# Kernel tuning notes

Measured on AMD Instinct MI355X. Metric: run time of the kernel, lower is better.

Reference implementation:

```python
import jax, jax.numpy as jnp
import numpy as np

B, C, H, W = 8, 256, 128, 128
SH, SW = 8, 8            # stoken_size
HH, WW = H // SH, W // SW
NH = 8                   # num_heads
HD = C // NH             # head_dim = 32
KD = HD                  # key_dim (attn_ratio=1)
ATTN_SCALE = KD ** (-0.5)
AFF_SCALE = C ** (-0.5)


def unfold9(x):
    """x: (B,C,hh,ww) -> (B, hh*ww, C, 9); matches Unfold(3) + transpose/reshape."""
    b, c, hh, ww = x.shape
    xp = jnp.pad(x, ((0, 0), (0, 0), (1, 1), (1, 1)))
    p = jnp.stack([xp[:, :, dy:dy + hh, dx:dx + ww]
                   for dy in range(3) for dx in range(3)], axis=2)  # (B,C,9,hh,ww)
    return p.transpose(0, 3, 4, 1, 2).reshape(b, hh * ww, c, 9)


def fold9(y):
    """y: (B,C,9,hh,ww) -> (B,C,hh,ww); matches Fold(3) (conv_transpose with identity kernels)."""
    hh, ww = y.shape[-2:]
    yp = jnp.pad(y, ((0, 0), (0, 0), (0, 0), (1, 1), (1, 1)))
    out = 0.
    for dy in range(3):
        for dx in range(3):
            out = out + yp[:, :, dy * 3 + dx, 2 - dy:2 - dy + hh, 2 - dx:2 - dx + ww]
    return out


def attention(sf, w_qkv, w_pe, w_proj):
    """Attention module with attn_ratio=1 (Conv layers have act=False, BN identity)."""
    b, c, hh, ww = sf.shape
    n = hh * ww
    qkv = jnp.einsum('oc,bchw->bohw', w_qkv, sf).reshape(b, NH, 2 * KD + HD, n)
    q, k, v = jnp.split(qkv, [KD, 2 * KD], axis=2)
    attn = jax.nn.softmax(jnp.einsum('bhkn,bhkm->bhnm', q, k) * ATTN_SCALE, axis=-1)
    o = jnp.einsum('bhdm,bhnm->bhdn', v, attn).reshape(b, c, hh, ww)
    pe = jax.lax.conv_general_dilated(
        v.reshape(b, c, hh, ww), w_pe, (1, 1), ((1, 1), (1, 1)),
        dimension_numbers=('NCHW', 'OIHW', 'NCHW'), feature_group_count=c)
    return jnp.einsum('oc,bchw->bohw', w_proj, o + pe)


def setup_inputs() -> dict:
    key = jax.random.key(0)
    k0, k1, k2, k3 = jax.random.split(key, 4)
    x = jax.random.normal(k0, (B, C, H, W), dtype=jnp.float32)
    w_qkv = jax.random.normal(k1, (3 * C, C), dtype=jnp.float32) * 0.05
    w_pe = jax.random.normal(k2, (C, 1, 3, 3), dtype=jnp.float32) * 0.05
    w_proj = jax.random.normal(k3, (C, C), dtype=jnp.float32) * 0.05
    return {'x': x, 'w_qkv': w_qkv, 'w_pe': w_pe, 'w_proj': w_proj}


def reference(x, w_qkv, w_pe, w_proj):
    # H,W divisible by stoken_size -> no padding branch
    xb = x.reshape(B, C, HH, SH, WW, SW)
    stoken = xb.mean(axis=(3, 5))                                   # (B,C,hh,ww) adaptive_avg_pool2d
    pix = xb.transpose(0, 2, 4, 3, 5, 1).reshape(B, HH * WW, SH * SW, C)
    # --- single no-grad iteration (n_iter=1) ---
    sf9 = unfold9(stoken)                                            # (B,n,C,9)
    aff = jax.nn.softmax(jnp.einsum('bnpc,bnck->bnpk', pix, sf9) * AFF_SCALE, axis=-1)
    aff = jax.lax.stop_gradient(aff)                                 # torch.no_grad
    asum = aff.sum(axis=2).transpose(0, 2, 1).reshape(B, 1, 9, HH, WW)
    asum = jax.lax.stop_gradient(fold9(asum))                        # (B,1,hh,ww)
    # --- super-token aggregation ---
    sf = jnp.einsum('bnpc,bnpk->bnck', pix, aff)                     # (B,n,C,9)
    sf = fold9(sf.transpose(0, 2, 3, 1).reshape(B, C, 9, HH, WW))    # (B,C,hh,ww)
    sf = sf / (asum + 1e-12)
    # --- refine with attention ---
    sf = attention(sf, w_qkv, w_pe, w_proj)
    # --- scatter back to pixels ---
    sf9b = unfold9(sf)                                               # (B,n,C,9)
    pix_out = jnp.einsum('bnck,bnpk->bnpc', sf9b, aff)               # (B,n,h*w,C)
    return pix_out.reshape(B, HH, WW, C, SH, SW).transpose(0, 3, 1, 4, 2, 5).reshape(B, C, H, W)
```

## Files before the change

kernel.cpp:

```cpp
#include <hip/hip_runtime.h>
#include <cstdint>
#include <cstddef>


#define AFF_SCALE 0.0625f
#define ATTN_SCALE 0.17677669529663687f

__global__ __launch_bounds__(128) void stoken_kernel(
    const float* __restrict__ x, float* __restrict__ stok_pad)
{
    int blk = blockIdx.x;
    int i  = blk & 15;
    int bc = blk >> 4;
    int t  = threadIdx.x;
    const float* xr = x + ((size_t)bc * 128 + i * 8) * 128 + t;
    float s = 0.f;
#pragma unroll
    for (int r = 0; r < 8; ++r) s += xr[r * 128];
    s += __shfl_down(s, 4, 64);
    s += __shfl_down(s, 2, 64);
    s += __shfl_down(s, 1, 64);
    if ((t & 7) == 0) {
        int j = t >> 3;
        int b = bc >> 8, c = bc & 255;
        stok_pad[(((size_t)b * 18 + (i + 1)) * 18 + (j + 1)) * 256 + c] =
            s * (1.f / 64.f);
    }
}

__global__ __launch_bounds__(256) void aff_agg_kernel(
    const float* __restrict__ x, const float* __restrict__ stok_pad,
    float* __restrict__ aff_g, float* __restrict__ asum_g,
    float* __restrict__ agg)
{
    __shared__ __align__(16) float pixs[256 * 68];
    __shared__ __align__(16) float sfs[9 * 260];
    __shared__ __align__(16) float part[576];

    int bid  = blockIdx.x;
    int xcd  = bid & 7, slot_ = bid >> 3;
    int pair = xcd * 128 + (slot_ >> 1);
    int m = pair & 7, i = (pair >> 3) & 15, b = pair >> 7;
    int j = m * 2 + (slot_ & 1);
    int bn = b * 256 + i * 16 + j;
    int t = threadIdx.x;

    {
        int c0 = t >> 3, pi = t & 7;
#pragma unroll
        for (int it = 0; it < 8; ++it) {
            int c = c0 + 32 * it;
            const float* xp = x + (((size_t)b * 256 + c) * 128 + i * 8 + pi) * 128 + j * 8;
            float4 f0 = *(const float4*)&xp[0];
            float4 f1 = *(const float4*)&xp[4];
            int gma = (c >> 2) & 3;
            int s0 = (2 * pi) ^ gma, s1 = (2 * pi + 1) ^ gma;
            *(float4*)&pixs[c * 68 + s0 * 4] = f0;
            *(float4*)&pixs[c * 68 + s1 * 4] = f1;
        }
    }
    {
        const float* spT = stok_pad + (size_t)b * 324 * 256;
#pragma unroll
        for (int dy = 0; dy < 3; ++dy)
#pragma unroll
            for (int dx = 0; dx < 3; ++dx)
                sfs[(dy * 3 + dx) * 260 + t] =
                    spT[((size_t)(i + dy) * 18 + (j + dx)) * 256 + t];
    }
    part[t] = 0.f;
    part[t + 256] = 0.f;
    if (t < 64) part[t + 512] = 0.f;
    __syncthreads();

    int w = t >> 6, l = t & 63;

    {
        int pq = l >> 2, cgl = l & 3;
        int cbase = w * 64 + cgl * 16;
        float acc[4][9];
#pragma unroll
        for (int ii = 0; ii < 4; ++ii)
#pragma unroll
            for (int k = 0; k < 9; ++k) acc[ii][k] = 0.f;

#pragma unroll
        for (int c4i = 0; c4i < 4; ++c4i) {
            int c = cbase + c4i * 4;
            int slot = (pq ^ c4i) * 4;
            const float4 p0 = *(const float4*)&pixs[(c + 0) * 68 + slot];
            const float4 p1 = *(const float4*)&pixs[(c + 1) * 68 + slot];
            const float4 p2 = *(const float4*)&pixs[(c + 2) * 68 + slot];
            const float4 p3 = *(const float4*)&pixs[(c + 3) * 68 + slot];
#pragma unroll
            for (int k = 0; k < 9; ++k) {
                const float4 sv = *(const float4*)&sfs[k * 260 + c];
                acc[0][k] += p0.x * sv.x + p1.x * sv.y + p2.x * sv.z + p3.x * sv.w;
                acc[1][k] += p0.y * sv.x + p1.y * sv.y + p2.y * sv.z + p3.y * sv.w;
                acc[2][k] += p0.z * sv.x + p1.z * sv.y + p2.z * sv.z + p3.z * sv.w;
                acc[3][k] += p0.w * sv.x + p1.w * sv.y + p2.w * sv.z + p3.w * sv.w;
            }
        }
#pragma unroll
        for (int ii = 0; ii < 4; ++ii)
#pragma unroll
            for (int k = 0; k < 9; ++k) {
                acc[ii][k] += __shfl_xor(acc[ii][k], 1, 64);
                acc[ii][k] += __shfl_xor(acc[ii][k], 2, 64);
            }
#pragma unroll
        for (int k = 0; k < 9; ++k) {
            float v01 = (cgl & 1) ? acc[1][k] : acc[0][k];
            float v23 = (cgl & 1) ? acc[3][k] : acc[2][k];
            float vk  = (cgl & 2) ? v23 : v01;
            atomicAdd(&part[l * 9 + k], vk);
        }
    }
    __syncthreads();

    float* affs = sfs;

    if (t < 64) {
        float a[9];
        float mx = -1e30f;
#pragma unroll
        for (int k = 0; k < 9; ++k) {
            float v = part[t * 9 + k] * AFF_SCALE;
            a[k] = v;
            mx = fmaxf(mx, v);
        }
        float ssum = 0.f;
#pragma unroll
        for (int k = 0; k < 9; ++k) { a[k] = __expf(a[k] - mx); ssum += a[k]; }
        float inv = 1.f / ssum;
#pragma unroll
        for (int k = 0; k < 9; ++k) {
            a[k] *= inv;
            affs[k * 64 + t] = a[k];
            aff_g[(size_t)bn * 576 + k * 64 + t] = a[k];
        }
#pragma unroll
        for (int k = 0; k < 9; ++k) {
            float r = a[k];
            r += __shfl_down(r, 32, 64); r += __shfl_down(r, 16, 64);
            r += __shfl_down(r, 8, 64);  r += __shfl_down(r, 4, 64);
            r += __shfl_down(r, 2, 64);  r += __shfl_down(r, 1, 64);
            if (t == 0) asum_g[(size_t)bn * 9 + k] = r;
        }
    }
    __syncthreads();

    {
        int cql = l >> 2, pq2 = l & 3;
        int cb2 = w * 64 + cql * 4;
        int gma = cql & 3;
        float acc2[4][9];
#pragma unroll
        for (int ii = 0; ii < 4; ++ii)
#pragma unroll
            for (int k = 0; k < 9; ++k) acc2[ii][k] = 0.f;

#pragma unroll
        for (int pp = 0; pp < 4; ++pp) {
            int p4 = pq2 * 4 + pp;
            int slot = (p4 ^ gma) * 4;
            const float4 q0 = *(const float4*)&pixs[(cb2 + 0) * 68 + slot];
            const float4 q1 = *(const float4*)&pixs[(cb2 + 1) * 68 + slot];
            const float4 q2 = *(const float4*)&pixs[(cb2 + 2) * 68 + slot];
            const float4 q3 = *(const float4*)&pixs[(cb2 + 3) * 68 + slot];
#pragma unroll
            for (int k = 0; k < 9; ++k) {
                const float4 av = *(const float4*)&affs[k * 64 + p4 * 4];
                acc2[0][k] += q0.x * av.x + q0.y * av.y + q0.z * av.z + q0.w * av.w;
                acc2[1][k] += q1.x * av.x + q1.y * av.y + q1.z * av.z + q1.w * av.w;
                acc2[2][k] += q2.x * av.x + q2.y * av.y + q2.z * av.z + q2.w * av.w;
                acc2[3][k] += q3.x * av.x + q3.y * av.y + q3.z * av.z + q3.w * av.w;
            }
        }
#pragma unroll
        for (int ii = 0; ii < 4; ++ii)
#pragma unroll
            for (int k = 0; k < 9; ++k) {
                acc2[ii][k] += __shfl_xor(acc2[ii][k], 1, 64);
                acc2[ii][k] += __shfl_xor(acc2[ii][k], 2, 64);
            }
        int cout = w * 64 + l;
#pragma unroll
        for (int k = 0; k < 9; ++k) {
            float v01 = (pq2 & 1) ? acc2[1][k] : acc2[0][k];
            float v23 = (pq2 & 1) ? acc2[3][k] : acc2[2][k];
            float vk  = (pq2 & 2) ? v23 : v01;
            agg[((size_t)bn * 9 + k) * 256 + cout] = vk;
        }
    }
}

__global__ __launch_bounds__(256) void fold_div_kernel(
    const float* __restrict__ agg, const float* __restrict__ asum_g,
    float* __restrict__ sf)
{
    __shared__ float v[256 * 17];
    int b = blockIdx.x >> 4, y = blockIdx.x & 15;
    int t = threadIdx.x;
    for (int x = 0; x < 16; ++x) {
        float af = 0.f, val = 0.f;
#pragma unroll
        for (int dy = 0; dy < 3; ++dy)
#pragma unroll
            for (int dx = 0; dx < 3; ++dx) {
                int ii = y + 1 - dy, jj = x + 1 - dx;
                if ((unsigned)ii < 16u && (unsigned)jj < 16u) {
                    int idx = (b * 256 + ii * 16 + jj) * 9 + dy * 3 + dx;
                    af  += asum_g[idx];
                    val += agg[(size_t)idx * 256 + t];
                }
            }
        v[t * 17 + x] = val / (af + 1e-12f);
    }
    __syncthreads();
    int xw = t & 15, cw0 = t >> 4;
#pragma unroll
    for (int it = 0; it < 16; ++it) {
        int c = cw0 + it * 16;
        sf[((size_t)b * 256 + c) * 256 + y * 16 + xw] = v[c * 17 + xw];
    }
}

__global__ __launch_bounds__(256) void gemm_w(
    const float* __restrict__ A, const float* __restrict__ Bm,
    float* __restrict__ Cout, int M, int mode)
{
    __shared__ float As[32 * 68];
    __shared__ float Bs[32 * 64];
    int b = blockIdx.x, o0 = blockIdx.y * 64, n0 = blockIdx.z * 64;
    int t = threadIdx.x;
    int tr = t >> 4, tc = t & 15;
    const float* Bb = Bm + (size_t)b * 256 * 256;
    float acc[4][4];
#pragma unroll
    for (int ii = 0; ii < 4; ++ii)
#pragma unroll
        for (int jj = 0; jj < 4; ++jj) acc[ii][jj] = 0.f;

    for (int k0 = 0; k0 < 256; k0 += 32) {
        {
            int ol = t >> 2, kq = (t & 3) * 8;
            const float* Ap = A + (size_t)(o0 + ol) * 256 + k0 + kq;
            const float4 f0 = *(const float4*)&Ap[0];
            const float4 f1 = *(const float4*)&Ap[4];
            As[(kq + 0) * 68 + ol] = f0.x; As[(kq + 1) * 68 + ol] = f0.y;
            As[(kq + 2) * 68 + ol] = f0.z; As[(kq + 3) * 68 + ol] = f0.w;
            As[(kq + 4) * 68 + ol] = f1.x; As[(kq + 5) * 68 + ol] = f1.y;
            As[(kq + 6) * 68 + ol] = f1.z; As[(kq + 7) * 68 + ol] = f1.w;
        }
#pragma unroll
        for (int i2 = 0; i2 < 8; ++i2) {
            int e = t + i2 * 256;
            int kl = e >> 6, nl = e & 63;
            Bs[kl * 64 + nl] = Bb[(size_t)(k0 + kl) * 256 + n0 + nl];
        }
        __syncthreads();
#pragma unroll
        for (int kk = 0; kk < 32; ++kk) {
            const float4 av = *(const float4*)&As[kk * 68 + tr * 4];
            const float4 bv = *(const float4*)&Bs[kk * 64 + tc * 4];
            acc[0][0] += av.x * bv.x; acc[0][1] += av.x * bv.y; acc[0][2] += av.x * bv.z; acc[0][3] += av.x * bv.w;
            acc[1][0] += av.y * bv.x; acc[1][1] += av.y * bv.y; acc[1][2] += av.y * bv.z; acc[1][3] += av.y * bv.w;
            acc[2][0] += av.z * bv.x; acc[2][1] += av.z * bv.y; acc[2][2] += av.z * bv.z; acc[2][3] += av.z * bv.w;
            acc[3][0] += av.w * bv.x; acc[3][1] += av.w * bv.y; acc[3][2] += av.w * bv.z; acc[3][3] += av.w * bv.w;
        }
        __syncthreads();
    }

    if (mode == 0) {
#pragma unroll
        for (int ii = 0; ii < 4; ++ii) {
            int o = o0 + tr * 4 + ii;
            float4 st = make_float4(acc[ii][0], acc[ii][1], acc[ii][2], acc[ii][3]);
            *(float4*)&Cout[((size_t)b * M + o) * 256 + n0 + tc * 4] = st;
        }
    } else {
#pragma unroll
        for (int jj = 0; jj < 4; ++jj) {
            int n = n0 + tc * 4 + jj;
            int y = n >> 4, x = n & 15;
            float4 st = make_float4(acc[0][jj], acc[1][jj], acc[2][jj], acc[3][jj]);
            *(float4*)&Cout[(((size_t)b * 18 + 1 + y) * 18 + 1 + x) * 256 + o0 + tr * 4] = st;
        }
    }
}

__global__ __launch_bounds__(256) void attn_kernel(
    const float* __restrict__ qkv, float* __restrict__ o_attn)
{
    __shared__ float smem[9216];
    int b = blockIdx.x, h = blockIdx.y, nt = blockIdx.z;
    int t = threadIdx.x, nl = t & 63, mq = t >> 6;
    int n = nt * 64 + nl;

    {
        int dd = t >> 3, mb = (t & 7) * 32;
        const float* krow = qkv + ((size_t)b * 768 + h * 96 + 32 + dd) * 256;
#pragma unroll
        for (int e4 = 0; e4 < 8; ++e4) {
            int m = mb + e4 * 4;
            const float4 kw = *(const float4*)&krow[m];
            smem[(m + 0) * 32 + dd] = kw.x; smem[(m + 1) * 32 + dd] = kw.y;
            smem[(m + 2) * 32 + dd] = kw.z; smem[(m + 3) * 32 + dd] = kw.w;
        }
    }
    float q[32];
    {
        const float* qbase = qkv + ((size_t)b * 768 + h * 96) * 256 + n;
#pragma unroll
        for (int d = 0; d < 32; ++d) q[d] = qbase[(size_t)d * 256];
    }
    __syncthreads();

    float l[64];
#pragma unroll
    for (int e = 0; e < 64; ++e) {
        const float* kp = &smem[(mq * 64 + e) * 32];
        float s = 0.f;
#pragma unroll
        for (int d4 = 0; d4 < 8; ++d4) {
            const float4 kv4 = *(const float4*)&kp[d4 * 4];
            s += q[d4 * 4 + 0] * kv4.x + q[d4 * 4 + 1] * kv4.y +
                 q[d4 * 4 + 2] * kv4.z + q[d4 * 4 + 3] * kv4.w;
        }
        l[e] = s * ATTN_SCALE;
    }
    float mx = -1e30f;
#pragma unroll
    for (int e = 0; e < 64; ++e) mx = fmaxf(mx, l[e]);
    float sm = 0.f;
#pragma unroll
    for (int e = 0; e < 64; ++e) { l[e] = __expf(l[e] - mx); sm += l[e]; }
    __syncthreads();

    {
        int dd = t >> 3, mb = (t & 7) * 32;
        const float* vrow = qkv + ((size_t)b * 768 + h * 96 + 64 + dd) * 256;
#pragma unroll
        for (int e4 = 0; e4 < 8; ++e4) {
            int m = mb + e4 * 4;
            const float4 vw = *(const float4*)&vrow[m];
            smem[(m + 0) * 32 + dd] = vw.x; smem[(m + 1) * 32 + dd] = vw.y;
            smem[(m + 2) * 32 + dd] = vw.z; smem[(m + 3) * 32 + dd] = vw.w;
        }
    }
    __syncthreads();

    float oa[32];
#pragma unroll
    for (int d = 0; d < 32; ++d) oa[d] = 0.f;
#pragma unroll
    for (int e = 0; e < 64; ++e) {
        float pm = l[e];
        const float* vp = &smem[(mq * 64 + e) * 32];
#pragma unroll
        for (int d4 = 0; d4 < 8; ++d4) {
            const float4 vv = *(const float4*)&vp[d4 * 4];
            oa[d4 * 4 + 0] += pm * vv.x; oa[d4 * 4 + 1] += pm * vv.y;
            oa[d4 * 4 + 2] += pm * vv.z; oa[d4 * 4 + 3] += pm * vv.w;
        }
    }
    __syncthreads();

    float* op   = smem;
    float* mxsm = smem + 8448;
    {
        int idx = mq * 64 + nl;
#pragma unroll
        for (int d = 0; d < 32; ++d) op[idx * 33 + d] = oa[d];
        mxsm[idx * 2 + 0] = mx;
        mxsm[idx * 2 + 1] = sm;
    }
    __syncthreads();

    if (t < 64) {
        float M2 = -1e30f;
#pragma unroll
        for (int q4 = 0; q4 < 4; ++q4) M2 = fmaxf(M2, mxsm[(q4 * 64 + t) * 2]);
        float w[4], S = 0.f;
#pragma unroll
        for (int q4 = 0; q4 < 4; ++q4) {
            w[q4] = __expf(mxsm[(q4 * 64 + t) * 2] - M2);
            S += mxsm[(q4 * 64 + t) * 2 + 1] * w[q4];
        }
        float inv = 1.f / S;
#pragma unroll
        for (int d = 0; d < 32; ++d) {
            float o = 0.f;
#pragma unroll
            for (int q4 = 0; q4 < 4; ++q4) o += op[(q4 * 64 + t) * 33 + d] * w[q4];
            o_attn[((size_t)b * 256 + h * 32 + d) * 256 + nt * 64 + t] = o * inv;
        }
    }
}

__global__ __launch_bounds__(256) void peadd_kernel(
    const float* __restrict__ qkv, const float* __restrict__ w_pe,
    float* __restrict__ o_attn)
{
    int bc = blockIdx.x;
    int b = bc >> 8, c = bc & 255;
    int t = threadIdx.x;
    int y = t >> 4, x = t & 15;
    int h = c >> 5, d = c & 31;
    const float* v = qkv + ((size_t)b * 768 + h * 96 + 64 + d) * 256;
    float acc = o_attn[(size_t)bc * 256 + t];
#pragma unroll
    for (int ky = 0; ky < 3; ++ky)
#pragma unroll
        for (int kx = 0; kx < 3; ++kx) {
            int yy = y + ky - 1, xx = x + kx - 1;
            if ((unsigned)yy < 16u && (unsigned)xx < 16u)
                acc += w_pe[c * 9 + ky * 3 + kx] * v[yy * 16 + xx];
        }
    o_attn[(size_t)bc * 256 + t] = acc;
}

__global__ __launch_bounds__(256) void scatter_kernel(
    const float* __restrict__ sfa_pad, const float* __restrict__ aff_g,
    float* __restrict__ out)
{
    __shared__ float ss[3 * 18 * 40];
    __shared__ float aff_s[16 * 577];

    int blk = blockIdx.x;
    int pi = blk & 7, i = (blk >> 3) & 15, b = blk >> 7;
    int t = threadIdx.x;

    for (int e = t; e < 1728; e += 256) {
        int dy = e / 576, rem = e % 576;
        int col = rem >> 5, idx = rem & 31;
        int q = idx >> 3, d = idx & 7;
        ss[(dy * 18 + col) * 40 + idx] =
            sfa_pad[(((size_t)b * 18 + i + dy) * 18 + col) * 256 + q * 64 + pi * 8 + d];
    }
    {
        const float* ag = aff_g + ((size_t)b * 256 + i * 16) * 576;
        for (int e = t; e < 9216; e += 256) {
            int j = e / 576, rem = e % 576;
            int k = rem >> 6, p = rem & 63;
            aff_s[j * 577 + p * 9 + k] = ag[j * 576 + rem];
        }
    }
    __syncthreads();

    int lane = t & 63, w = t >> 6;
    int j0 = lane >> 3, pj = lane & 7;
    int j1 = j0 + 8;

    float S0[4][9], S1[4][9];
#pragma unroll
    for (int q = 0; q < 4; ++q)
#pragma unroll
        for (int k = 0; k < 9; ++k) {
            int dy = k / 3, dx = k % 3;
            S0[q][k] = ss[(dy * 18 + j0 + dx) * 40 + q * 8 + pj];
            S1[q][k] = ss[(dy * 18 + j1 + dx) * 40 + q * 8 + pj];
        }

    int y = i * 8 + pi;
    size_t ob = (size_t)b * 256 * 16384 + (size_t)y * 128;
    const float* A0 = &aff_s[j0 * 577];
    const float* A1 = &aff_s[j1 * 577];
    for (int p = w * 16; p < w * 16 + 16; ++p) {
        float a0[9], a1[9];
#pragma unroll
        for (int k = 0; k < 9; ++k) { a0[k] = A0[p * 9 + k]; a1[k] = A1[p * 9 + k]; }
#pragma unroll
        for (int q = 0; q < 4; ++q) {
            int c2 = p * 4 + q;
            float v0 = 0.f, v1 = 0.f;
#pragma unroll
            for (int k = 0; k < 9; ++k) {
                v0 += S0[q][k] * a0[k];
                v1 += S1[q][k] * a1[k];
            }
            out[ob + (size_t)c2 * 16384 + lane] = v0;
            out[ob + (size_t)c2 * 16384 + 64 + lane] = v1;
        }
    }
}

extern "C" void kernel_launch(void* const* d_in, const int* in_sizes, int n_in,
                              void* d_out, int out_size, void* d_ws, size_t ws_size,
                              hipStream_t stream) {
    const float* x      = (const float*)d_in[0];
    const float* w_qkv  = (const float*)d_in[1];
    const float* w_pe   = (const float*)d_in[2];
    const float* w_proj = (const float*)d_in[3];
    float* out = (float*)d_out;
    float* agg = (float*)d_out;

    float* ws = (float*)d_ws;
    const size_t o_aff  = 0;
    const size_t o_asum = 1179648;
    const size_t o_pad  = 1198080;
    const size_t o_sf   = 1861632;
    const size_t o_qkv  = 2385920;

    hipMemsetAsync(ws + o_pad, 0, 663552 * sizeof(float), stream);

    stoken_kernel<<<8 * 256 * 16, 128, 0, stream>>>(x, ws + o_pad);
    aff_agg_kernel<<<8 * 256, 256, 0, stream>>>(x, ws + o_pad, ws + o_aff,
                                                ws + o_asum, agg);
    fold_div_kernel<<<8 * 16, 256, 0, stream>>>(agg, ws + o_asum, ws + o_sf);
    gemm_w<<<dim3(8, 12, 4), 256, 0, stream>>>(w_qkv, ws + o_sf, ws + o_qkv, 768, 0);
    hipMemsetAsync(ws + o_pad, 0, 663552 * sizeof(float), stream);
    attn_kernel<<<dim3(8, 8, 4), 256, 0, stream>>>(ws + o_qkv, ws + o_sf);
    peadd_kernel<<<8 * 256, 256, 0, stream>>>(ws + o_qkv, w_pe, ws + o_sf);
    gemm_w<<<dim3(8, 4, 4), 256, 0, stream>>>(w_proj, ws + o_sf, ws + o_pad, 256, 1);
    scatter_kernel<<<8 * 16 * 8, 256, 0, stream>>>(ws + o_pad, ws + o_aff, out);
}
```

Measured before the change: 442.9 us.

## Split affinity/aggregation kernel, read pixels from global, drop pad memsets

The fused affinity+aggregation kernel is split into two kernels that each read pixel data directly from global memory instead of staging a 68KB shared tile, with launch bounds requesting 4 blocks per SM to raise occupancy. The two memsets of the padded buffer are removed and replaced by bounds checks on the halo reads in the affinity and scatter kernels. Cross-lane reductions use DPP intrinsics instead of shuffles. The trade-off is that x is read twice from global/L2 and there is one extra kernel launch.

New measurement: 442.1 us. Within noise of the previous version (-0.2%).

```diff
diff --git a/kernel.cpp b/kernel.cpp
--- a/kernel.cpp
+++ b/kernel.cpp
@@ -5,6 +5,15 @@
 
 #define AFF_SCALE 0.0625f
 #define ATTN_SCALE 0.17677669529663687f
+
+__device__ __forceinline__ float dpp_add_xor1(float v) {
+    int p = __builtin_amdgcn_update_dpp(0, __float_as_int(v), 0xB1, 0xF, 0xF, true);
+    return v + __int_as_float(p);
+}
+__device__ __forceinline__ float dpp_add_xor2(float v) {
+    int p = __builtin_amdgcn_update_dpp(0, __float_as_int(v), 0x4E, 0xF, 0xF, true);
+    return v + __int_as_float(p);
+}
 
 __global__ __launch_bounds__(128) void stoken_kernel(
     const float* __restrict__ x, float* __restrict__ stok_pad)
@@ -28,12 +37,10 @@
     }
 }
 
-__global__ __launch_bounds__(256) void aff_agg_kernel(
+__global__ __launch_bounds__(256, 4) void aff_kernel(
     const float* __restrict__ x, const float* __restrict__ stok_pad,
-    float* __restrict__ aff_g, float* __restrict__ asum_g,
-    float* __restrict__ agg)
-{
-    __shared__ __align__(16) float pixs[256 * 68];
+    float* __restrict__ aff_g, float* __restrict__ asum_g)
+{
     __shared__ __align__(16) float sfs[9 * 260];
     __shared__ __align__(16) float part[576];
 
@@ -46,27 +53,17 @@
     int t = threadIdx.x;
 
     {
-        int c0 = t >> 3, pi = t & 7;
-#pragma unroll
-        for (int it = 0; it < 8; ++it) {
-            int c = c0 + 32 * it;
-            const float* xp = x + (((size_t)b * 256 + c) * 128 + i * 8 + pi) * 128 + j * 8;
-            float4 f0 = *(const float4*)&xp[0];
-            float4 f1 = *(const float4*)&xp[4];
-            int gma = (c >> 2) & 3;
-            int s0 = (2 * pi) ^ gma, s1 = (2 * pi + 1) ^ gma;
-            *(float4*)&pixs[c * 68 + s0 * 4] = f0;
-            *(float4*)&pixs[c * 68 + s1 * 4] = f1;
-        }
-    }
-    {
         const float* spT = stok_pad + (size_t)b * 324 * 256;
 #pragma unroll
         for (int dy = 0; dy < 3; ++dy)
 #pragma unroll
-            for (int dx = 0; dx < 3; ++dx)
-                sfs[(dy * 3 + dx) * 260 + t] =
-                    spT[((size_t)(i + dy) * 18 + (j + dx)) * 256 + t];
+            for (int dx = 0; dx < 3; ++dx) {
+                int r = i + dy, cn = j + dx;
+                float v = 0.f;
+                if ((unsigned)(r - 1) < 16u && (unsigned)(cn - 1) < 16u)
+                    v = spT[((size_t)r * 18 + cn) * 256 + t];
+                sfs[(dy * 3 + dx) * 260 + t] = v;
+            }
     }
     part[t] = 0.f;
     part[t + 256] = 0.f;
@@ -74,10 +71,12 @@
     __syncthreads();
 
     int w = t >> 6, l = t & 63;
-
     {
         int pq = l >> 2, cgl = l & 3;
         int cbase = w * 64 + cgl * 16;
+        int pi = pq >> 1, pj4 = (pq & 1) * 4;
+        const float* xb = x + (size_t)(b * 256) * 16384
+                            + (size_t)(i * 8 + pi) * 128 + j * 8 + pj4;
         float acc[4][9];
 #pragma unroll
         for (int ii = 0; ii < 4; ++ii)
@@ -87,11 +86,10 @@
 #pragma unroll
         for (int c4i = 0; c4i < 4; ++c4i) {
             int c = cbase + c4i * 4;
-            int slot = (pq ^ c4i) * 4;
-            const float4 p0 = *(const float4*)&pixs[(c + 0) * 68 + slot];
-            const float4 p1 = *(const float4*)&pixs[(c + 1) * 68 + slot];
-            const float4 p2 = *(const float4*)&pixs[(c + 2) * 68 + slot];
-            const float4 p3 = *(const float4*)&pixs[(c + 3) * 68 + slot];
+            const float4 p0 = *(const float4*)&xb[(size_t)(c + 0) * 16384];
+            const float4 p1 = *(const float4*)&xb[(size_t)(c + 1) * 16384];
+            const float4 p2 = *(const float4*)&xb[(size_t)(c + 2) * 16384];
+            const float4 p3 = *(const float4*)&xb[(size_t)(c + 3) * 16384];
 #pragma unroll
             for (int k = 0; k < 9; ++k) {
                 const float4 sv = *(const float4*)&sfs[k * 260 + c];
@@ -105,8 +103,8 @@
         for (int ii = 0; ii < 4; ++ii)
 #pragma unroll
             for (int k = 0; k < 9; ++k) {
-                acc[ii][k] += __shfl_xor(acc[ii][k], 1, 64);
-                acc[ii][k] += __shfl_xor(acc[ii][k], 2, 64);
+                acc[ii][k] = dpp_add_xor1(acc[ii][k]);
+                acc[ii][k] = dpp_add_xor2(acc[ii][k]);
             }
 #pragma unroll
         for (int k = 0; k < 9; ++k) {
@@ -118,8 +116,6 @@
     }
     __syncthreads();
 
-    float* affs = sfs;
-
     if (t < 64) {
         float a[9];
         float mx = -1e30f;
@@ -136,7 +132,6 @@
 #pragma unroll
         for (int k = 0; k < 9; ++k) {
             a[k] *= inv;
-            affs[k * 64 + t] = a[k];
             aff_g[(size_t)bn * 576 + k * 64 + t] = a[k];
         }
 #pragma unroll
@@ -148,50 +143,72 @@
             if (t == 0) asum_g[(size_t)bn * 9 + k] = r;
         }
     }
-    __syncthreads();
-
-    {
-        int cql = l >> 2, pq2 = l & 3;
-        int cb2 = w * 64 + cql * 4;
-        int gma = cql & 3;
-        float acc2[4][9];
-#pragma unroll
-        for (int ii = 0; ii < 4; ++ii)
-#pragma unroll
-            for (int k = 0; k < 9; ++k) acc2[ii][k] = 0.f;
-
-#pragma unroll
-        for (int pp = 0; pp < 4; ++pp) {
-            int p4 = pq2 * 4 + pp;
-            int slot = (p4 ^ gma) * 4;
-            const float4 q0 = *(const float4*)&pixs[(cb2 + 0) * 68 + slot];
-            const float4 q1 = *(const float4*)&pixs[(cb2 + 1) * 68 + slot];
-            const float4 q2 = *(const float4*)&pixs[(cb2 + 2) * 68 + slot];
-            const float4 q3 = *(const float4*)&pixs[(cb2 + 3) * 68 + slot];
-#pragma unroll
-            for (int k = 0; k < 9; ++k) {
-                const float4 av = *(const float4*)&affs[k * 64 + p4 * 4];
-                acc2[0][k] += q0.x * av.x + q0.y * av.y + q0.z * av.z + q0.w * av.w;
-                acc2[1][k] += q1.x * av.x + q1.y * av.y + q1.z * av.z + q1.w * av.w;
-                acc2[2][k] += q2.x * av.x + q2.y * av.y + q2.z * av.z + q2.w * av.w;
-                acc2[3][k] += q3.x * av.x + q3.y * av.y + q3.z * av.z + q3.w * av.w;
-            }
-        }
-#pragma unroll
-        for (int ii = 0; ii < 4; ++ii)
-#pragma unroll
-            for (int k = 0; k < 9; ++k) {
-                acc2[ii][k] += __shfl_xor(acc2[ii][k], 1, 64);
-                acc2[ii][k] += __shfl_xor(acc2[ii][k], 2, 64);
-            }
-        int cout = w * 64 + l;
-#pragma unroll
-        for (int k = 0; k < 9; ++k) {
-            float v01 = (pq2 & 1) ? acc2[1][k] : acc2[0][k];
-            float v23 = (pq2 & 1) ? acc2[3][k] : acc2[2][k];
-            float vk  = (pq2 & 2) ? v23 : v01;
-            agg[((size_t)bn * 9 + k) * 256 + cout] = vk;
-        }
+}
+
+__global__ __launch_bounds__(256, 4) void agg_kernel(
+    const float* __restrict__ x, const float* __restrict__ aff_g,
+    float* __restrict__ agg)
+{
+    __shared__ __align__(16) float affs[9 * 64];
+
+    int bid  = blockIdx.x;
+    int xcd  = bid & 7, slot_ = bid >> 3;
+    int pair = xcd * 128 + (slot_ >> 1);
+    int m = pair & 7, i = (pair >> 3) & 15, b = pair >> 7;
+    int j = m * 2 + (slot_ & 1);
+    int bn = b * 256 + i * 16 + j;
+    int t = threadIdx.x;
+
+    {
+        const float* ag = aff_g + (size_t)bn * 576;
+        affs[t] = ag[t];
+        affs[t + 256] = ag[t + 256];
+        if (t < 64) affs[t + 512] = ag[t + 512];
+    }
+    __syncthreads();
+
+    int w = t >> 6, l = t & 63;
+    int cql = l >> 2, pq2 = l & 3;
+    int cb2 = w * 64 + cql * 4;
+    const float* xb = x + (size_t)(b * 256) * 16384 + (size_t)(i * 8) * 128 + j * 8;
+    float acc2[4][9];
+#pragma unroll
+    for (int ii = 0; ii < 4; ++ii)
+#pragma unroll
+        for (int k = 0; k < 9; ++k) acc2[ii][k] = 0.f;
+
+#pragma unroll
+    for (int pp = 0; pp < 4; ++pp) {
+        int p4 = pq2 * 4 + pp;
+        int pi = p4 >> 1, pj4 = (p4 & 1) * 4;
+        const float* xr = xb + (size_t)pi * 128 + pj4;
+        const float4 q0 = *(const float4*)&xr[(size_t)(cb2 + 0) * 16384];
+        const float4 q1 = *(const float4*)&xr[(size_t)(cb2 + 1) * 16384];
+        const float4 q2 = *(const float4*)&xr[(size_t)(cb2 + 2) * 16384];
+        const float4 q3 = *(const float4*)&xr[(size_t)(cb2 + 3) * 16384];
+#pragma unroll
+        for (int k = 0; k < 9; ++k) {
+            const float4 av = *(const float4*)&affs[k * 64 + p4 * 4];
+            acc2[0][k] += q0.x * av.x + q0.y * av.y + q0.z * av.z + q0.w * av.w;
+            acc2[1][k] += q1.x * av.x + q1.y * av.y + q1.z * av.z + q1.w * av.w;
+            acc2[2][k] += q2.x * av.x + q2.y * av.y + q2.z * av.z + q2.w * av.w;
+            acc2[3][k] += q3.x * av.x + q3.y * av.y + q3.z * av.z + q3.w * av.w;
+        }
+    }
+#pragma unroll
+    for (int ii = 0; ii < 4; ++ii)
+#pragma unroll
+        for (int k = 0; k < 9; ++k) {
+            acc2[ii][k] = dpp_add_xor1(acc2[ii][k]);
+            acc2[ii][k] = dpp_add_xor2(acc2[ii][k]);
+        }
+    int cout = w * 64 + l;
+#pragma unroll
+    for (int k = 0; k < 9; ++k) {
+        float v01 = (pq2 & 1) ? acc2[1][k] : acc2[0][k];
+        float v23 = (pq2 & 1) ? acc2[3][k] : acc2[2][k];
+        float vk  = (pq2 & 2) ? v23 : v01;
+        agg[((size_t)bn * 9 + k) * 256 + cout] = vk;
     }
 }
 
@@ -436,8 +453,11 @@
         int dy = e / 576, rem = e % 576;
         int col = rem >> 5, idx = rem & 31;
         int q = idx >> 3, d = idx & 7;
-        ss[(dy * 18 + col) * 40 + idx] =
-            sfa_pad[(((size_t)b * 18 + i + dy) * 18 + col) * 256 + q * 64 + pi * 8 + d];
+        int row = i + dy;
+        float v = 0.f;
+        if ((unsigned)(row - 1) < 16u && (unsigned)(col - 1) < 16u)
+            v = sfa_pad[(((size_t)b * 18 + row) * 18 + col) * 256 + q * 64 + pi * 8 + d];
+        ss[(dy * 18 + col) * 40 + idx] = v;
     }
     {
         const float* ag = aff_g + ((size_t)b * 256 + i * 16) * 576;
@@ -503,14 +523,11 @@
     const size_t o_sf   = 1861632;
     const size_t o_qkv  = 2385920;
 
-    hipMemsetAsync(ws + o_pad, 0, 663552 * sizeof(float), stream);
-
     stoken_kernel<<<8 * 256 * 16, 128, 0, stream>>>(x, ws + o_pad);
-    aff_agg_kernel<<<8 * 256, 256, 0, stream>>>(x, ws + o_pad, ws + o_aff,
-                                                ws + o_asum, agg);
+    aff_kernel<<<8 * 256, 256, 0, stream>>>(x, ws + o_pad, ws + o_aff, ws + o_asum);
+    agg_kernel<<<8 * 256, 256, 0, stream>>>(x, ws + o_aff, agg);
     fold_div_kernel<<<8 * 16, 256, 0, stream>>>(agg, ws + o_asum, ws + o_sf);
     gemm_w<<<dim3(8, 12, 4), 256, 0, stream>>>(w_qkv, ws + o_sf, ws + o_qkv, 768, 0);
-    hipMemsetAsync(ws + o_pad, 0, 663552 * sizeof(float), stream);
     attn_kernel<<<dim3(8, 8, 4), 256, 0, stream>>>(ws + o_qkv, ws + o_sf);
     peadd_kernel<<<8 * 256, 256, 0, stream>>>(ws + o_qkv, w_pe, ws + o_sf);
     gemm_w<<<dim3(8, 4, 4), 256, 0, stream>>>(w_proj, ws + o_sf, ws + o_pad, 256, 1);
```
